# Kernel optimization log

Measured on AMD Instinct MI355X. Metric: run time of the kernel, lower is better.

## Reference

```python
import jax, jax.numpy as jnp
import numpy as np

RRELU_SLOPE = (1.0 / 8.0 + 1.0 / 3.0) / 2.0  # torch.rrelu eval-mode negative slope

N_NODES, N_EDGES, DIM, N_LAYERS = 10000, 640000, 128, 2


def setup_inputs() -> dict:
    key = jax.random.key(0)
    ks = jax.random.split(key, 7)
    scale = 1.0 / np.sqrt(DIM).astype(np.float32)
    return {
        "node_feats": jax.random.normal(ks[0], (N_NODES, DIM), jnp.float32),
        "edge_feats": jax.random.normal(ks[1], (N_EDGES, DIM), jnp.float32),
        "src": jax.random.randint(ks[2], (N_EDGES,), 0, N_NODES),
        "dst": jax.random.randint(ks[3], (N_EDGES,), 0, N_NODES),
        "W1": jax.random.normal(ks[4], (N_LAYERS, DIM, DIM), jnp.float32) * scale,
        "W2": jax.random.normal(ks[5], (N_LAYERS, DIM, DIM), jnp.float32) * scale,
        "W3": jax.random.normal(ks[6], (N_LAYERS, DIM, DIM), jnp.float32) * scale,
    }


def reference(node_feats, edge_feats, src, dst, W1, W2, W3):
    n_nodes = node_feats.shape[0]
    ones = jnp.ones((src.shape[0],), dtype=node_feats.dtype)
    deg = jax.ops.segment_sum(ones, dst, num_segments=n_nodes)  # in-degrees
    iso = (deg == 0)[:, None]                                   # isolated-node mask
    denom = jnp.maximum(deg, 1.0)[:, None]                      # safe mean divisor

    h = node_feats
    for l in range(W1.shape[0]):
        # per-edge message: linear1(src_h + edge_h)
        msg = (h[src] + edge_feats) @ W1[l]                     # (E, H)
        # mean-aggregate to destination nodes (0 for zero in-degree, as in dgl)
        neigh = jax.ops.segment_sum(msg, dst, num_segments=n_nodes) / denom
        # self-loop message; isolated nodes use linear3 instead of linear2
        self_msg = jnp.where(iso, h @ W3[l], h @ W2[l])
        x = neigh + self_msg
        h = jnp.where(x >= 0, x, RRELU_SLOPE * x)               # rrelu (eval mode)
    return h
```

## Files before the change

kernel.cpp:

```cpp
#include <hip/hip_runtime.h>

#define NN 10000
#define NE 640000
#define SLOPE 0.22916666666666666f

typedef float    f2v __attribute__((ext_vector_type(2)));
typedef float    f4v __attribute__((ext_vector_type(4)));
typedef unsigned u2v __attribute__((ext_vector_type(2)));
typedef unsigned u4v __attribute__((ext_vector_type(4)));

__device__ __forceinline__ float blo(unsigned v){ return __uint_as_float(v << 16); }
__device__ __forceinline__ float bhi(unsigned v){ return __uint_as_float(v & 0xffff0000u); }
__device__ __forceinline__ unsigned f2b(float x){
  unsigned u = __float_as_uint(x);
  return (u + 0x7fffu + ((u >> 16) & 1u)) >> 16;
}
__device__ __forceinline__ unsigned pack2(float a, float b){
  return f2b(a) | (f2b(b) << 16);
}
__device__ __forceinline__ float rrelu(float x){ return x >= 0.f ? x : x * SLOPE; }
__device__ __forceinline__ int clampi(int x, int hi){ return x < 0 ? 0 : (x > hi ? hi : x); }

__device__ __forceinline__ int detect_f32(const unsigned short* __restrict__ w1){
  int lane = threadIdx.x & 63;
  unsigned short u = w1[lane];
  int e = (u >> 7) & 0xFF;
  int pass = ((u & 0x7FFF) == 0 || (e >= 100 && e <= 135)) ? 1 : 0;
  unsigned long long b = __ballot(pass);
  return (__popcll(b) < 56) ? 1 : 0;
}

__device__ __forceinline__ float2 ld2(const void* p, long i, int f32){
  if (f32) return ((const float2*)p)[i];
  unsigned v = ((const unsigned*)p)[i];
  return make_float2(blo(v), bhi(v));
}
__device__ __forceinline__ void st2(void* p, long i, float2 v, int f32){
  if (f32) ((float2*)p)[i] = v;
  else ((unsigned*)p)[i] = pack2(v.x, v.y);
}

__global__ __launch_bounds__(256) void k_hist(const int* __restrict__ dst,
                                              int* __restrict__ deg){
  int i = blockIdx.x * 256 + threadIdx.x;
  if (i < NE) atomicAdd(&deg[clampi(dst[i], NN - 1)], 1);
}

__global__ __launch_bounds__(1024) void k_scan(const int* __restrict__ deg,
                                               int* __restrict__ row_ptr,
                                               int* __restrict__ cursor){
  __shared__ int part[1024];
  int t = threadIdx.x;
  int base = t * 10;
  int local[10];
  int s = 0;
  #pragma unroll
  for (int j = 0; j < 10; j++){
    int idx = base + j;
    int v = (idx < NN) ? deg[idx] : 0;
    local[j] = s; s += v;
  }
  part[t] = s;
  __syncthreads();
  for (int off = 1; off < 1024; off <<= 1){
    int v = (t >= off) ? part[t - off] : 0;
    __syncthreads();
    part[t] += v;
    __syncthreads();
  }
  int pre = (t == 0) ? 0 : part[t - 1];
  #pragma unroll
  for (int j = 0; j < 10; j++){
    int idx = base + j;
    if (idx < NN){ int rp = pre + local[j]; row_ptr[idx] = rp; cursor[idx] = rp; }
  }
  if (t == 1023) row_ptr[NN] = part[1023];
}

__global__ __launch_bounds__(256) void k_scatter_cast(const int* __restrict__ src,
                          const int* __restrict__ dst,
                          int* __restrict__ cursor,
                          unsigned long long* __restrict__ csr,
                          const void* __restrict__ nf, unsigned* __restrict__ nfbf,
                          const unsigned short* __restrict__ w1){
  int f32 = detect_f32(w1);
  int i = blockIdx.x * 256 + threadIdx.x;
  if (i >= NE) return;
  float2 v = ld2(nf, i, f32);
  nfbf[i] = pack2(v.x, v.y);
  int d = clampi(dst[i], NN - 1);
  int p = clampi(atomicAdd(&cursor[d], 1), NE - 1);
  csr[p] = ((unsigned long long)(unsigned)i << 32) | (unsigned)clampi(src[i], NN - 1);
}

__global__ __launch_bounds__(256) void k_agg0(const void* __restrict__ ef,
                                              const unsigned* __restrict__ nfbf,
                                              const int* __restrict__ row_ptr,
                                              const unsigned long long* __restrict__ csr,
                                              unsigned* __restrict__ eagg,
                                              unsigned* __restrict__ A,
                                              const unsigned short* __restrict__ w1){
  int f32 = detect_f32(w1);
  int wave = threadIdx.x >> 6, lane = threadIdx.x & 63;
  int n = blockIdx.x * 4 + wave;
  if (n >= NN) return;
  int beg = row_ptr[n], end = row_ptr[n + 1];
  float inv = 1.f / fmaxf((float)(end - beg), 1.f);
  int half = lane >> 5, sl = lane & 31;

  if (f32){
    const f4v* ef4 = (const f4v*)ef;
    const u2v* nf2 = (const u2v*)nfbf;
    float s0=0.f,s1=0.f,s2=0.f,s3=0.f;
    float h0=0.f,h1=0.f,h2=0.f,h3=0.f;
    int i = beg;
    for (; i + 8 <= end; i += 8){
      unsigned long long c[4];
      #pragma unroll
      for (int q = 0; q < 4; q++) c[q] = csr[i + 2*q + half];
      f4v v[4]; u2v hv[4];
      #pragma unroll
      for (int q = 0; q < 4; q++)
        v[q] = __builtin_nontemporal_load(ef4 + (long)(c[q] >> 32) * 32 + sl);
      #pragma unroll
      for (int q = 0; q < 4; q++)
        hv[q] = nf2[(long)(unsigned)(c[q] & 0xffffffffu) * 32 + sl];
      #pragma unroll
      for (int q = 0; q < 4; q++){
        s0 += v[q].x; s1 += v[q].y; s2 += v[q].z; s3 += v[q].w;
        h0 += blo(hv[q].x); h1 += bhi(hv[q].x);
        h2 += blo(hv[q].y); h3 += bhi(hv[q].y);
      }
    }
    for (; i + 2 <= end; i += 2){
      unsigned long long c = csr[i + half];
      f4v v = __builtin_nontemporal_load(ef4 + (long)(c >> 32) * 32 + sl);
      u2v hv = nf2[(long)(unsigned)(c & 0xffffffffu) * 32 + sl];
      s0 += v.x; s1 += v.y; s2 += v.z; s3 += v.w;
      h0 += blo(hv.x); h1 += bhi(hv.x); h2 += blo(hv.y); h3 += bhi(hv.y);
    }
    if (i < end && half == 0){
      unsigned long long c = csr[i];
      f4v v = __builtin_nontemporal_load(ef4 + (long)(c >> 32) * 32 + sl);
      u2v hv = nf2[(long)(unsigned)(c & 0xffffffffu) * 32 + sl];
      s0 += v.x; s1 += v.y; s2 += v.z; s3 += v.w;
      h0 += blo(hv.x); h1 += bhi(hv.x); h2 += blo(hv.y); h3 += bhi(hv.y);
    }
    s0 += __shfl_xor(s0, 32); s1 += __shfl_xor(s1, 32);
    s2 += __shfl_xor(s2, 32); s3 += __shfl_xor(s3, 32);
    h0 += __shfl_xor(h0, 32); h1 += __shfl_xor(h1, 32);
    h2 += __shfl_xor(h2, 32); h3 += __shfl_xor(h3, 32);
    if (half == 0){
      u2v eo; eo.x = pack2(s0, s1); eo.y = pack2(s2, s3);
      ((u2v*)eagg)[(long)n * 32 + sl] = eo;
      u2v ao; ao.x = pack2((s0 + h0) * inv, (s1 + h1) * inv);
      ao.y = pack2((s2 + h2) * inv, (s3 + h3) * inv);
      ((u2v*)A)[(long)n * 32 + sl] = ao;
    }
    return;
  }

  {
    const u2v* ef2 = (const u2v*)ef;
    const u2v* nf2 = (const u2v*)nfbf;
    float e00=0.f,e01=0.f,e10=0.f,e11=0.f;
    float h00=0.f,h01=0.f,h10=0.f,h11=0.f;
    int i = beg;
    for (; i + 8 <= end; i += 8){
      unsigned long long c[4];
      #pragma unroll
      for (int q = 0; q < 4; q++) c[q] = csr[i + 2*q + half];
      u2v v[4], hv[4];
      #pragma unroll
      for (int q = 0; q < 4; q++)
        v[q] = __builtin_nontemporal_load(ef2 + (long)(c[q] >> 32) * 32 + sl);
      #pragma unroll
      for (int q = 0; q < 4; q++)
        hv[q] = nf2[(long)(unsigned)(c[q] & 0xffffffffu) * 32 + sl];
      #pragma unroll
      for (int q = 0; q < 4; q++){
        e00 += blo(v[q].x);  e01 += bhi(v[q].x);
        e10 += blo(v[q].y);  e11 += bhi(v[q].y);
        h00 += blo(hv[q].x); h01 += bhi(hv[q].x);
        h10 += blo(hv[q].y); h11 += bhi(hv[q].y);
      }
    }
    for (; i + 2 <= end; i += 2){
      unsigned long long c = csr[i + half];
      u2v v = __builtin_nontemporal_load(ef2 + (long)(c >> 32) * 32 + sl);
      u2v hv = nf2[(long)(unsigned)(c & 0xffffffffu) * 32 + sl];
      e00 += blo(v.x);  e01 += bhi(v.x);  e10 += blo(v.y);  e11 += bhi(v.y);
      h00 += blo(hv.x); h01 += bhi(hv.x); h10 += blo(hv.y); h11 += bhi(hv.y);
    }
    if (i < end && half == 0){
      unsigned long long c = csr[i];
      u2v v = __builtin_nontemporal_load(ef2 + (long)(c >> 32) * 32 + sl);
      u2v hv = nf2[(long)(unsigned)(c & 0xffffffffu) * 32 + sl];
      e00 += blo(v.x);  e01 += bhi(v.x);  e10 += blo(v.y);  e11 += bhi(v.y);
      h00 += blo(hv.x); h01 += bhi(hv.x); h10 += blo(hv.y); h11 += bhi(hv.y);
    }
    e00 += __shfl_xor(e00, 32); e01 += __shfl_xor(e01, 32);
    e10 += __shfl_xor(e10, 32); e11 += __shfl_xor(e11, 32);
    h00 += __shfl_xor(h00, 32); h01 += __shfl_xor(h01, 32);
    h10 += __shfl_xor(h10, 32); h11 += __shfl_xor(h11, 32);
    if (half == 0){
      u2v eo; eo.x = pack2(e00, e01); eo.y = pack2(e10, e11);
      ((u2v*)eagg)[(long)n * 32 + sl] = eo;
      u2v ao; ao.x = pack2((e00 + h00) * inv, (e01 + h01) * inv);
      ao.y = pack2((e10 + h10) * inv, (e11 + h11) * inv);
      ((u2v*)A)[(long)n * 32 + sl] = ao;
    }
  }
}

__global__ __launch_bounds__(256) void k_agg_h(const unsigned* __restrict__ h,
                                               const int* __restrict__ row_ptr,
                                               const unsigned long long* __restrict__ csr,
                                               const unsigned* __restrict__ eagg,
                                               unsigned* __restrict__ A){
  int wave = threadIdx.x >> 6, lane = threadIdx.x & 63;
  int n = blockIdx.x * 4 + wave;
  if (n >= NN) return;
  int beg = row_ptr[n], end = row_ptr[n + 1];
  int qt = lane >> 4, ql = lane & 15;
  const u4v* h4 = (const u4v*)h;
  float a0=0.f,a1=0.f,a2=0.f,a3=0.f,a4=0.f,a5=0.f,a6=0.f,a7=0.f;
  int i = beg;
  for (; i + 16 <= end; i += 16){
    unsigned c[4];
    #pragma unroll
    for (int q = 0; q < 4; q++) c[q] = (unsigned)(csr[i + 4*q + qt] & 0xffffffffu);
    u4v v[4];
    #pragma unroll
    for (int q = 0; q < 4; q++) v[q] = h4[(long)c[q] * 16 + ql];
    #pragma unroll
    for (int q = 0; q < 4; q++){
      a0 += blo(v[q].x); a1 += bhi(v[q].x); a2 += blo(v[q].y); a3 += bhi(v[q].y);
      a4 += blo(v[q].z); a5 += bhi(v[q].z); a6 += blo(v[q].w); a7 += bhi(v[q].w);
    }
  }
  for (; i + 4 <= end; i += 4){
    unsigned c = (unsigned)(csr[i + qt] & 0xffffffffu);
    u4v v = h4[(long)c * 16 + ql];
    a0 += blo(v.x); a1 += bhi(v.x); a2 += blo(v.y); a3 += bhi(v.y);
    a4 += blo(v.z); a5 += bhi(v.z); a6 += blo(v.w); a7 += bhi(v.w);
  }
  int r = end - i;
  if (qt < r){
    unsigned c = (unsigned)(csr[i + qt] & 0xffffffffu);
    u4v v = h4[(long)c * 16 + ql];
    a0 += blo(v.x); a1 += bhi(v.x); a2 += blo(v.y); a3 += bhi(v.y);
    a4 += blo(v.z); a5 += bhi(v.z); a6 += blo(v.w); a7 += bhi(v.w);
  }
  a0 += __shfl_xor(a0, 16); a1 += __shfl_xor(a1, 16);
  a2 += __shfl_xor(a2, 16); a3 += __shfl_xor(a3, 16);
  a4 += __shfl_xor(a4, 16); a5 += __shfl_xor(a5, 16);
  a6 += __shfl_xor(a6, 16); a7 += __shfl_xor(a7, 16);
  a0 += __shfl_xor(a0, 32); a1 += __shfl_xor(a1, 32);
  a2 += __shfl_xor(a2, 32); a3 += __shfl_xor(a3, 32);
  a4 += __shfl_xor(a4, 32); a5 += __shfl_xor(a5, 32);
  a6 += __shfl_xor(a6, 32); a7 += __shfl_xor(a7, 32);
  if (qt == 0){
    u4v ev = ((const u4v*)eagg)[(long)n * 16 + ql];
    a0 += blo(ev.x); a1 += bhi(ev.x); a2 += blo(ev.y); a3 += bhi(ev.y);
    a4 += blo(ev.z); a5 += bhi(ev.z); a6 += blo(ev.w); a7 += bhi(ev.w);
    float inv = 1.f / fmaxf((float)(end - beg), 1.f);
    u4v ao;
    ao.x = pack2(a0 * inv, a1 * inv); ao.y = pack2(a2 * inv, a3 * inv);
    ao.z = pack2(a4 * inv, a5 * inv); ao.w = pack2(a6 * inv, a7 * inv);
    ((u4v*)A)[(long)n * 16 + ql] = ao;
  }
}

__global__ __launch_bounds__(512) void k_lin(const unsigned* __restrict__ A,
                                             const unsigned* __restrict__ H,
                                             const void* __restrict__ W1,
                                             const void* __restrict__ W2,
                                             const void* __restrict__ W3, long woff,
                                             const int* __restrict__ deg,
                                             void* __restrict__ out, int outmode){
  int f32 = detect_f32((const unsigned short*)W1);
  __shared__ unsigned lw[16384];
  int t = threadIdx.x;
  for (int i = t; i < 16384; i += 512){
    float2 v = (i < 8192) ? ld2(W1, woff + i, f32) : ld2(W2, woff + (i - 8192), f32);
    lw[i] = pack2(v.x, v.y);
  }
  __syncthreads();
  int wave = t >> 6, lane = t & 63;
  int nb = (blockIdx.x * 8 + wave) * 5;
  long base[5]; int valid[5];
  float a0[5], a1[5];
  #pragma unroll
  for (int j = 0; j < 5; ++j){
    int n = nb + j;
    valid[j] = (n < NN);
    base[j] = valid[j] ? (long)n * 64 : 0;
    a0[j] = 0.f; a1[j] = 0.f;
  }
  for (int kk = 0; kk < 64; ++kk){
    unsigned w1a = lw[(2 * kk) * 64 + lane];
    unsigned w1b = lw[(2 * kk + 1) * 64 + lane];
    unsigned w2a = lw[8192 + (2 * kk) * 64 + lane];
    unsigned w2b = lw[8192 + (2 * kk + 1) * 64 + lane];
    #pragma unroll
    for (int j = 0; j < 5; ++j){
      unsigned av = A[base[j] + kk];
      unsigned hv = H[base[j] + kk];
      float A0 = blo(av), A1 = bhi(av);
      float H0 = blo(hv), H1 = bhi(hv);
      a0[j] += A0 * blo(w1a) + A1 * blo(w1b) + H0 * blo(w2a) + H1 * blo(w2b);
      a1[j] += A0 * bhi(w1a) + A1 * bhi(w1b) + H0 * bhi(w2a) + H1 * bhi(w2b);
    }
  }
  #pragma unroll
  for (int j = 0; j < 5; ++j){
    if (valid[j] && deg[nb + j] == 0){
      float b0 = 0.f, b1 = 0.f;
      for (int kk = 0; kk < 64; ++kk){
        unsigned hv = H[base[j] + kk];
        float H0 = blo(hv), H1 = bhi(hv);
        float2 wa = ld2(W3, woff + (long)(2 * kk) * 64 + lane, f32);
        float2 wb = ld2(W3, woff + (long)(2 * kk + 1) * 64 + lane, f32);
        b0 += H0 * wa.x + H1 * wb.x;
        b1 += H0 * wa.y + H1 * wb.y;
      }
      a0[j] = b0; a1[j] = b1;
    }
  }
  #pragma unroll
  for (int j = 0; j < 5; ++j){
    if (!valid[j]) continue;
    float r0 = rrelu(a0[j]), r1 = rrelu(a1[j]);
    if (outmode) st2(out, base[j] + lane, make_float2(r0, r1), f32);
    else ((unsigned*)out)[base[j] + lane] = pack2(r0, r1);
  }
}

extern "C" void kernel_launch(void* const* d_in, const int* in_sizes, int n_in,
                              void* d_out, int out_size, void* d_ws, size_t ws_size,
                              hipStream_t stream) {
  const void* nf  = d_in[0];
  const void* ef  = d_in[1];
  const int*  src = (const int*)d_in[2];
  const int*  dst = (const int*)d_in[3];
  const void* W1  = d_in[4];
  const void* W2  = d_in[5];
  const void* W3  = d_in[6];

  char* w = (char*)d_ws;
  int* deg      = (int*)(w + 4096);
  int* row_ptr  = (int*)(w + 49152);
  int* cursor   = (int*)(w + 94208);
  unsigned long long* csr = (unsigned long long*)(w + 139264);
  unsigned* eagg = (unsigned*)(w + 5259264);
  unsigned* Abuf = (unsigned*)(w + 7819264);
  unsigned* nfbf = (unsigned*)(w + 10379264);
  unsigned* h1   = (unsigned*)(w + 12939264);

  const long WOFF1 = 8192;
  const unsigned short* w1u = (const unsigned short*)W1;

  hipMemsetAsync(deg, 0, NN * sizeof(int), stream);
  k_hist<<<2500, 256, 0, stream>>>(dst, deg);
  k_scan<<<1, 1024, 0, stream>>>(deg, row_ptr, cursor);
  k_scatter_cast<<<2500, 256, 0, stream>>>(src, dst, cursor, csr, nf, nfbf, w1u);
  k_agg0<<<2500, 256, 0, stream>>>(ef, nfbf, row_ptr, csr, eagg, Abuf, w1u);

  k_lin<<<250, 512, 0, stream>>>(Abuf, nfbf, W1, W2, W3, 0L, deg, h1, 0);

  k_agg_h<<<2500, 256, 0, stream>>>(h1, row_ptr, csr, eagg, Abuf);
  k_lin<<<250, 512, 0, stream>>>(Abuf, h1, W1, W2, W3, WOFF1, deg, d_out, 1);
}
```

Measured before the change: 625.3 us.

## Fuse per-layer aggregation with the linear transform and prepack weights to bf16

```diff
diff --git a/kernel.cpp b/kernel.cpp
--- a/kernel.cpp
+++ b/kernel.cpp
@@ -40,10 +40,24 @@
   else ((unsigned*)p)[i] = pack2(v.x, v.y);
 }
 
-__global__ __launch_bounds__(256) void k_hist(const int* __restrict__ dst,
-                                              int* __restrict__ deg){
+__global__ __launch_bounds__(256) void k_hist_pack(const int* __restrict__ dst,
+                          int* __restrict__ deg,
+                          const void* __restrict__ W1, const void* __restrict__ W2,
+                          const void* __restrict__ W3, unsigned* __restrict__ wpk,
+                          const unsigned short* __restrict__ w1u){
+  int f32 = detect_f32(w1u);
   int i = blockIdx.x * 256 + threadIdx.x;
   if (i < NE) atomicAdd(&deg[clampi(dst[i], NN - 1)], 1);
+  if (i < 49152){
+    float2 v;
+    if (i < 8192)       v = ld2(W1, i, f32);
+    else if (i < 16384) v = ld2(W2, i - 8192, f32);
+    else if (i < 24576) v = ld2(W1, 8192 + (i - 16384), f32);
+    else if (i < 32768) v = ld2(W2, 8192 + (i - 24576), f32);
+    else if (i < 40960) v = ld2(W3, i - 32768, f32);
+    else                v = ld2(W3, 8192 + (i - 40960), f32);
+    wpk[i] = pack2(v.x, v.y);
+  }
 }
 
 __global__ __launch_bounds__(1024) void k_scan(const int* __restrict__ deg,
@@ -93,220 +107,128 @@
   csr[p] = ((unsigned long long)(unsigned)i << 32) | (unsigned)clampi(src[i], NN - 1);
 }
 
-__global__ __launch_bounds__(256) void k_agg0(const void* __restrict__ ef,
-                                              const unsigned* __restrict__ nfbf,
-                                              const int* __restrict__ row_ptr,
-                                              const unsigned long long* __restrict__ csr,
-                                              unsigned* __restrict__ eagg,
-                                              unsigned* __restrict__ A,
-                                              const unsigned short* __restrict__ w1){
-  int f32 = detect_f32(w1);
+__global__ __launch_bounds__(256) void k_fused0(const void* __restrict__ ef,
+                          const unsigned* __restrict__ nfbf,
+                          const int* __restrict__ row_ptr,
+                          const unsigned long long* __restrict__ csr,
+                          unsigned* __restrict__ eagg,
+                          const unsigned* __restrict__ wpk,
+                          const int* __restrict__ deg,
+                          unsigned* __restrict__ h1,
+                          const unsigned short* __restrict__ w1u){
+  int f32 = detect_f32(w1u);
+  __shared__ unsigned sA[4][4][64];
   int wave = threadIdx.x >> 6, lane = threadIdx.x & 63;
-  int n = blockIdx.x * 4 + wave;
-  if (n >= NN) return;
-  int beg = row_ptr[n], end = row_ptr[n + 1];
-  float inv = 1.f / fmaxf((float)(end - beg), 1.f);
   int half = lane >> 5, sl = lane & 31;
-
-  if (f32){
-    const f4v* ef4 = (const f4v*)ef;
+  int nb = (blockIdx.x * 4 + wave) * 4;
+
+  for (int j = 0; j < 4; ++j){
+    int n = nb + j;
+    int beg = row_ptr[n], end = row_ptr[n + 1];
+    float inv = 1.f / fmaxf((float)(end - beg), 1.f);
+    float s0=0.f,s1=0.f,s2=0.f,s3=0.f;
+    float h0=0.f,h1v=0.f,h2=0.f,h3=0.f;
     const u2v* nf2 = (const u2v*)nfbf;
-    float s0=0.f,s1=0.f,s2=0.f,s3=0.f;
-    float h0=0.f,h1=0.f,h2=0.f,h3=0.f;
-    int i = beg;
-    for (; i + 8 <= end; i += 8){
-      unsigned long long c[4];
-      #pragma unroll
-      for (int q = 0; q < 4; q++) c[q] = csr[i + 2*q + half];
-      f4v v[4]; u2v hv[4];
-      #pragma unroll
-      for (int q = 0; q < 4; q++)
-        v[q] = __builtin_nontemporal_load(ef4 + (long)(c[q] >> 32) * 32 + sl);
-      #pragma unroll
-      for (int q = 0; q < 4; q++)
-        hv[q] = nf2[(long)(unsigned)(c[q] & 0xffffffffu) * 32 + sl];
-      #pragma unroll
-      for (int q = 0; q < 4; q++){
-        s0 += v[q].x; s1 += v[q].y; s2 += v[q].z; s3 += v[q].w;
-        h0 += blo(hv[q].x); h1 += bhi(hv[q].x);
-        h2 += blo(hv[q].y); h3 += bhi(hv[q].y);
-      }
-    }
-    for (; i + 2 <= end; i += 2){
-      unsigned long long c = csr[i + half];
-      f4v v = __builtin_nontemporal_load(ef4 + (long)(c >> 32) * 32 + sl);
-      u2v hv = nf2[(long)(unsigned)(c & 0xffffffffu) * 32 + sl];
-      s0 += v.x; s1 += v.y; s2 += v.z; s3 += v.w;
-      h0 += blo(hv.x); h1 += bhi(hv.x); h2 += blo(hv.y); h3 += bhi(hv.y);
-    }
-    if (i < end && half == 0){
-      unsigned long long c = csr[i];
-      f4v v = __builtin_nontemporal_load(ef4 + (long)(c >> 32) * 32 + sl);
-      u2v hv = nf2[(long)(unsigned)(c & 0xffffffffu) * 32 + sl];
-      s0 += v.x; s1 += v.y; s2 += v.z; s3 += v.w;
-      h0 += blo(hv.x); h1 += bhi(hv.x); h2 += blo(hv.y); h3 += bhi(hv.y);
+
+    if (f32){
+      const f4v* ef4 = (const f4v*)ef;
+      int i = beg;
+      for (; i + 8 <= end; i += 8){
+        unsigned long long c[4];
+        #pragma unroll
+        for (int q = 0; q < 4; q++) c[q] = csr[i + 2*q + half];
+        f4v v[4]; u2v hv[4];
+        #pragma unroll
+        for (int q = 0; q < 4; q++)
+          v[q] = __builtin_nontemporal_load(ef4 + (long)(c[q] >> 32) * 32 + sl);
+        #pragma unroll
+        for (int q = 0; q < 4; q++)
+          hv[q] = nf2[(long)(unsigned)(c[q] & 0xffffffffu) * 32 + sl];
+        #pragma unroll
+        for (int q = 0; q < 4; q++){
+          s0 += v[q].x; s1 += v[q].y; s2 += v[q].z; s3 += v[q].w;
+          h0 += blo(hv[q].x); h1v += bhi(hv[q].x);
+          h2 += blo(hv[q].y); h3  += bhi(hv[q].y);
+        }
+      }
+      for (; i + 2 <= end; i += 2){
+        unsigned long long c = csr[i + half];
+        f4v v = __builtin_nontemporal_load(ef4 + (long)(c >> 32) * 32 + sl);
+        u2v hv = nf2[(long)(unsigned)(c & 0xffffffffu) * 32 + sl];
+        s0 += v.x; s1 += v.y; s2 += v.z; s3 += v.w;
+        h0 += blo(hv.x); h1v += bhi(hv.x); h2 += blo(hv.y); h3 += bhi(hv.y);
+      }
+      if (i < end && half == 0){
+        unsigned long long c = csr[i];
+        f4v v = __builtin_nontemporal_load(ef4 + (long)(c >> 32) * 32 + sl);
+        u2v hv = nf2[(long)(unsigned)(c & 0xffffffffu) * 32 + sl];
+        s0 += v.x; s1 += v.y; s2 += v.z; s3 += v.w;
+        h0 += blo(hv.x); h1v += bhi(hv.x); h2 += blo(hv.y); h3 += bhi(hv.y);
+      }
+    } else {
+      const u2v* ef2 = (const u2v*)ef;
+      int i = beg;
+      for (; i + 8 <= end; i += 8){
+        unsigned long long c[4];
+        #pragma unroll
+        for (int q = 0; q < 4; q++) c[q] = csr[i + 2*q + half];
+        u2v v[4], hv[4];
+        #pragma unroll
+        for (int q = 0; q < 4; q++)
+          v[q] = __builtin_nontemporal_load(ef2 + (long)(c[q] >> 32) * 32 + sl);
+        #pragma unroll
+        for (int q = 0; q < 4; q++)
+          hv[q] = nf2[(long)(unsigned)(c[q] & 0xffffffffu) * 32 + sl];
+        #pragma unroll
+        for (int q = 0; q < 4; q++){
+          s0 += blo(v[q].x);  s1 += bhi(v[q].x);
+          s2 += blo(v[q].y);  s3 += bhi(v[q].y);
+          h0 += blo(hv[q].x); h1v += bhi(hv[q].x);
+          h2 += blo(hv[q].y); h3  += bhi(hv[q].y);
+        }
+      }
+      for (; i + 2 <= end; i += 2){
+        unsigned long long c = csr[i + half];
+        u2v v = __builtin_nontemporal_load(ef2 + (long)(c >> 32) * 32 + sl);
+        u2v hv = nf2[(long)(unsigned)(c & 0xffffffffu) * 32 + sl];
+        s0 += blo(v.x); s1 += bhi(v.x); s2 += blo(v.y); s3 += bhi(v.y);
+        h0 += blo(hv.x); h1v += bhi(hv.x); h2 += blo(hv.y); h3 += bhi(hv.y);
+      }
+      if (i < end && half == 0){
+        unsigned long long c = csr[i];
+        u2v v = __builtin_nontemporal_load(ef2 + (long)(c >> 32) * 32 + sl);
+        u2v hv = nf2[(long)(unsigned)(c & 0xffffffffu) * 32 + sl];
+        s0 += blo(v.x); s1 += bhi(v.x); s2 += blo(v.y); s3 += bhi(v.y);
+        h0 += blo(hv.x); h1v += bhi(hv.x); h2 += blo(hv.y); h3 += bhi(hv.y);
+      }
     }
     s0 += __shfl_xor(s0, 32); s1 += __shfl_xor(s1, 32);
     s2 += __shfl_xor(s2, 32); s3 += __shfl_xor(s3, 32);
-    h0 += __shfl_xor(h0, 32); h1 += __shfl_xor(h1, 32);
-    h2 += __shfl_xor(h2, 32); h3 += __shfl_xor(h3, 32);
+    h0 += __shfl_xor(h0, 32); h1v += __shfl_xor(h1v, 32);
+    h2 += __shfl_xor(h2, 32); h3  += __shfl_xor(h3, 32);
     if (half == 0){
       u2v eo; eo.x = pack2(s0, s1); eo.y = pack2(s2, s3);
       ((u2v*)eagg)[(long)n * 32 + sl] = eo;
-      u2v ao; ao.x = pack2((s0 + h0) * inv, (s1 + h1) * inv);
+      u2v ao; ao.x = pack2((s0 + h0) * inv, (s1 + h1v) * inv);
       ao.y = pack2((s2 + h2) * inv, (s3 + h3) * inv);
-      ((u2v*)A)[(long)n * 32 + sl] = ao;
-    }
-    return;
-  }
-
-  {
-    const u2v* ef2 = (const u2v*)ef;
-    const u2v* nf2 = (const u2v*)nfbf;
-    float e00=0.f,e01=0.f,e10=0.f,e11=0.f;
-    float h00=0.f,h01=0.f,h10=0.f,h11=0.f;
-    int i = beg;
-    for (; i + 8 <= end; i += 8){
-      unsigned long long c[4];
-      #pragma unroll
-      for (int q = 0; q < 4; q++) c[q] = csr[i + 2*q + half];
-      u2v v[4], hv[4];
-      #pragma unroll
-      for (int q = 0; q < 4; q++)
-        v[q] = __builtin_nontemporal_load(ef2 + (long)(c[q] >> 32) * 32 + sl);
-      #pragma unroll
-      for (int q = 0; q < 4; q++)
-        hv[q] = nf2[(long)(unsigned)(c[q] & 0xffffffffu) * 32 + sl];
-      #pragma unroll
-      for (int q = 0; q < 4; q++){
-        e00 += blo(v[q].x);  e01 += bhi(v[q].x);
-        e10 += blo(v[q].y);  e11 += bhi(v[q].y);
-        h00 += blo(hv[q].x); h01 += bhi(hv[q].x);
-        h10 += blo(hv[q].y); h11 += bhi(hv[q].y);
-      }
-    }
-    for (; i + 2 <= end; i += 2){
-      unsigned long long c = csr[i + half];
-      u2v v = __builtin_nontemporal_load(ef2 + (long)(c >> 32) * 32 + sl);
-      u2v hv = nf2[(long)(unsigned)(c & 0xffffffffu) * 32 + sl];
-      e00 += blo(v.x);  e01 += bhi(v.x);  e10 += blo(v.y);  e11 += bhi(v.y);
-      h00 += blo(hv.x); h01 += bhi(hv.x); h10 += blo(hv.y); h11 += bhi(hv.y);
-    }
-    if (i < end && half == 0){
-      unsigned long long c = csr[i];
-      u2v v = __builtin_nontemporal_load(ef2 + (long)(c >> 32) * 32 + sl);
-      u2v hv = nf2[(long)(unsigned)(c & 0xffffffffu) * 32 + sl];
-      e00 += blo(v.x);  e01 += bhi(v.x);  e10 += blo(v.y);  e11 += bhi(v.y);
-      h00 += blo(hv.x); h01 += bhi(hv.x); h10 += blo(hv.y); h11 += bhi(hv.y);
-    }
-    e00 += __shfl_xor(e00, 32); e01 += __shfl_xor(e01, 32);
-    e10 += __shfl_xor(e10, 32); e11 += __shfl_xor(e11, 32);
-    h00 += __shfl_xor(h00, 32); h01 += __shfl_xor(h01, 32);
-    h10 += __shfl_xor(h10, 32); h11 += __shfl_xor(h11, 32);
-    if (half == 0){
-      u2v eo; eo.x = pack2(e00, e01); eo.y = pack2(e10, e11);
-      ((u2v*)eagg)[(long)n * 32 + sl] = eo;
-      u2v ao; ao.x = pack2((e00 + h00) * inv, (e01 + h01) * inv);
-      ao.y = pack2((e10 + h10) * inv, (e11 + h11) * inv);
-      ((u2v*)A)[(long)n * 32 + sl] = ao;
-    }
-  }
-}
-
-__global__ __launch_bounds__(256) void k_agg_h(const unsigned* __restrict__ h,
-                                               const int* __restrict__ row_ptr,
-                                               const unsigned long long* __restrict__ csr,
-                                               const unsigned* __restrict__ eagg,
-                                               unsigned* __restrict__ A){
-  int wave = threadIdx.x >> 6, lane = threadIdx.x & 63;
-  int n = blockIdx.x * 4 + wave;
-  if (n >= NN) return;
-  int beg = row_ptr[n], end = row_ptr[n + 1];
-  int qt = lane >> 4, ql = lane & 15;
-  const u4v* h4 = (const u4v*)h;
-  float a0=0.f,a1=0.f,a2=0.f,a3=0.f,a4=0.f,a5=0.f,a6=0.f,a7=0.f;
-  int i = beg;
-  for (; i + 16 <= end; i += 16){
-    unsigned c[4];
+      *(u2v*)&sA[wave][j][2 * sl] = ao;
+    }
+  }
+
+  long hb[4]; float a0[4], a1[4];
+  #pragma unroll
+  for (int j = 0; j < 4; ++j){ hb[j] = (long)(nb + j) * 64; a0[j] = 0.f; a1[j] = 0.f; }
+  const unsigned* wp1 = wpk;
+  const unsigned* wp2 = wpk + 8192;
+  for (int kk = 0; kk < 64; ++kk){
+    unsigned w1a = wp1[(2 * kk) * 64 + lane];
+    unsigned w1b = wp1[(2 * kk + 1) * 64 + lane];
+    unsigned w2a = wp2[(2 * kk) * 64 + lane];
+    unsigned w2b = wp2[(2 * kk + 1) * 64 + lane];
     #pragma unroll
-    for (int q = 0; q < 4; q++) c[q] = (unsigned)(csr[i + 4*q + qt] & 0xffffffffu);
-    u4v v[4];
-    #pragma unroll
-    for (int q = 0; q < 4; q++) v[q] = h4[(long)c[q] * 16 + ql];
-    #pragma unroll
-    for (int q = 0; q < 4; q++){
-      a0 += blo(v[q].x); a1 += bhi(v[q].x); a2 += blo(v[q].y); a3 += bhi(v[q].y);
-      a4 += blo(v[q].z); a5 += bhi(v[q].z); a6 += blo(v[q].w); a7 += bhi(v[q].w);
-    }
-  }
-  for (; i + 4 <= end; i += 4){
-    unsigned c = (unsigned)(csr[i + qt] & 0xffffffffu);
-    u4v v = h4[(long)c * 16 + ql];
-    a0 += blo(v.x); a1 += bhi(v.x); a2 += blo(v.y); a3 += bhi(v.y);
-    a4 += blo(v.z); a5 += bhi(v.z); a6 += blo(v.w); a7 += bhi(v.w);
-  }
-  int r = end - i;
-  if (qt < r){
-    unsigned c = (unsigned)(csr[i + qt] & 0xffffffffu);
-    u4v v = h4[(long)c * 16 + ql];
-    a0 += blo(v.x); a1 += bhi(v.x); a2 += blo(v.y); a3 += bhi(v.y);
-    a4 += blo(v.z); a5 += bhi(v.z); a6 += blo(v.w); a7 += bhi(v.w);
-  }
-  a0 += __shfl_xor(a0, 16); a1 += __shfl_xor(a1, 16);
-  a2 += __shfl_xor(a2, 16); a3 += __shfl_xor(a3, 16);
-  a4 += __shfl_xor(a4, 16); a5 += __shfl_xor(a5, 16);
-  a6 += __shfl_xor(a6, 16); a7 += __shfl_xor(a7, 16);
-  a0 += __shfl_xor(a0, 32); a1 += __shfl_xor(a1, 32);
-  a2 += __shfl_xor(a2, 32); a3 += __shfl_xor(a3, 32);
-  a4 += __shfl_xor(a4, 32); a5 += __shfl_xor(a5, 32);
-  a6 += __shfl_xor(a6, 32); a7 += __shfl_xor(a7, 32);
-  if (qt == 0){
-    u4v ev = ((const u4v*)eagg)[(long)n * 16 + ql];
-    a0 += blo(ev.x); a1 += bhi(ev.x); a2 += blo(ev.y); a3 += bhi(ev.y);
-    a4 += blo(ev.z); a5 += bhi(ev.z); a6 += blo(ev.w); a7 += bhi(ev.w);
-    float inv = 1.f / fmaxf((float)(end - beg), 1.f);
-    u4v ao;
-    ao.x = pack2(a0 * inv, a1 * inv); ao.y = pack2(a2 * inv, a3 * inv);
-    ao.z = pack2(a4 * inv, a5 * inv); ao.w = pack2(a6 * inv, a7 * inv);
-    ((u4v*)A)[(long)n * 16 + ql] = ao;
-  }
-}
-
-__global__ __launch_bounds__(512) void k_lin(const unsigned* __restrict__ A,
-                                             const unsigned* __restrict__ H,
-                                             const void* __restrict__ W1,
-                                             const void* __restrict__ W2,
-                                             const void* __restrict__ W3, long woff,
-                                             const int* __restrict__ deg,
-                                             void* __restrict__ out, int outmode){
-  int f32 = detect_f32((const unsigned short*)W1);
-  __shared__ unsigned lw[16384];
-  int t = threadIdx.x;
-  for (int i = t; i < 16384; i += 512){
-    float2 v = (i < 8192) ? ld2(W1, woff + i, f32) : ld2(W2, woff + (i - 8192), f32);
-    lw[i] = pack2(v.x, v.y);
-  }
-  __syncthreads();
-  int wave = t >> 6, lane = t & 63;
-  int nb = (blockIdx.x * 8 + wave) * 5;
-  long base[5]; int valid[5];
-  float a0[5], a1[5];
-  #pragma unroll
-  for (int j = 0; j < 5; ++j){
-    int n = nb + j;
-    valid[j] = (n < NN);
-    base[j] = valid[j] ? (long)n * 64 : 0;
-    a0[j] = 0.f; a1[j] = 0.f;
-  }
-  for (int kk = 0; kk < 64; ++kk){
-    unsigned w1a = lw[(2 * kk) * 64 + lane];
-    unsigned w1b = lw[(2 * kk + 1) * 64 + lane];
-    unsigned w2a = lw[8192 + (2 * kk) * 64 + lane];
-    unsigned w2b = lw[8192 + (2 * kk + 1) * 64 + lane];
-    #pragma unroll
-    for (int j = 0; j < 5; ++j){
-      unsigned av = A[base[j] + kk];
-      unsigned hv = H[base[j] + kk];
+    for (int j = 0; j < 4; ++j){
+      unsigned av = sA[wave][j][kk];
+      unsigned hv = nfbf[hb[j] + kk];
       float A0 = blo(av), A1 = bhi(av);
       float H0 = blo(hv), H1 = bhi(hv);
       a0[j] += A0 * blo(w1a) + A1 * blo(w1b) + H0 * blo(w2a) + H1 * blo(w2b);
@@ -314,27 +236,129 @@
     }
   }
   #pragma unroll
-  for (int j = 0; j < 5; ++j){
-    if (valid[j] && deg[nb + j] == 0){
+  for (int j = 0; j < 4; ++j){
+    if (deg[nb + j] == 0){
+      const unsigned* wp3 = wpk + 32768;
       float b0 = 0.f, b1 = 0.f;
       for (int kk = 0; kk < 64; ++kk){
-        unsigned hv = H[base[j] + kk];
-        float H0 = blo(hv), H1 = bhi(hv);
-        float2 wa = ld2(W3, woff + (long)(2 * kk) * 64 + lane, f32);
-        float2 wb = ld2(W3, woff + (long)(2 * kk + 1) * 64 + lane, f32);
-        b0 += H0 * wa.x + H1 * wb.x;
-        b1 += H0 * wa.y + H1 * wb.y;
+        unsigned hv = nfbf[hb[j] + kk];
+        unsigned wa = wp3[(2 * kk) * 64 + lane];
+        unsigned wb = wp3[(2 * kk + 1) * 64 + lane];
+        b0 += blo(hv) * blo(wa) + bhi(hv) * blo(wb);
+        b1 += blo(hv) * bhi(wa) + bhi(hv) * bhi(wb);
       }
       a0[j] = b0; a1[j] = b1;
     }
   }
   #pragma unroll
-  for (int j = 0; j < 5; ++j){
-    if (!valid[j]) continue;
-    float r0 = rrelu(a0[j]), r1 = rrelu(a1[j]);
-    if (outmode) st2(out, base[j] + lane, make_float2(r0, r1), f32);
-    else ((unsigned*)out)[base[j] + lane] = pack2(r0, r1);
-  }
+  for (int j = 0; j < 4; ++j)
+    h1[hb[j] + lane] = pack2(rrelu(a0[j]), rrelu(a1[j]));
+}
+
+__global__ __launch_bounds__(256) void k_fused1(const unsigned* __restrict__ h1,
+                          const int* __restrict__ row_ptr,
+                          const unsigned long long* __restrict__ csr,
+                          const unsigned* __restrict__ eagg,
+                          const unsigned* __restrict__ wpk,
+                          const int* __restrict__ deg,
+                          void* __restrict__ out,
+                          const unsigned short* __restrict__ w1u){
+  int f32 = detect_f32(w1u);
+  __shared__ unsigned sA[4][4][64];
+  int wave = threadIdx.x >> 6, lane = threadIdx.x & 63;
+  int qt = lane >> 4, ql = lane & 15;
+  int nb = (blockIdx.x * 4 + wave) * 4;
+  const u4v* h4 = (const u4v*)h1;
+
+  for (int j = 0; j < 4; ++j){
+    int n = nb + j;
+    int beg = row_ptr[n], end = row_ptr[n + 1];
+    float a0=0.f,a1=0.f,a2=0.f,a3=0.f,a4=0.f,a5=0.f,a6=0.f,a7=0.f;
+    int i = beg;
+    for (; i + 16 <= end; i += 16){
+      unsigned c[4];
+      #pragma unroll
+      for (int q = 0; q < 4; q++) c[q] = (unsigned)(csr[i + 4*q + qt] & 0xffffffffu);
+      u4v v[4];
+      #pragma unroll
+      for (int q = 0; q < 4; q++) v[q] = h4[(long)c[q] * 16 + ql];
+      #pragma unroll
+      for (int q = 0; q < 4; q++){
+        a0 += blo(v[q].x); a1 += bhi(v[q].x); a2 += blo(v[q].y); a3 += bhi(v[q].y);
+        a4 += blo(v[q].z); a5 += bhi(v[q].z); a6 += blo(v[q].w); a7 += bhi(v[q].w);
+      }
+    }
+    for (; i + 4 <= end; i += 4){
+      unsigned c = (unsigned)(csr[i + qt] & 0xffffffffu);
+      u4v v = h4[(long)c * 16 + ql];
+      a0 += blo(v.x); a1 += bhi(v.x); a2 += blo(v.y); a3 += bhi(v.y);
+      a4 += blo(v.z); a5 += bhi(v.z); a6 += blo(v.w); a7 += bhi(v.w);
+    }
+    int r = end - i;
+    if (qt < r){
+      unsigned c = (unsigned)(csr[i + qt] & 0xffffffffu);
+      u4v v = h4[(long)c * 16 + ql];
+      a0 += blo(v.x); a1 += bhi(v.x); a2 += blo(v.y); a3 += bhi(v.y);
+      a4 += blo(v.z); a5 += bhi(v.z); a6 += blo(v.w); a7 += bhi(v.w);
+    }
+    a0 += __shfl_xor(a0, 16); a1 += __shfl_xor(a1, 16);
+    a2 += __shfl_xor(a2, 16); a3 += __shfl_xor(a3, 16);
+    a4 += __shfl_xor(a4, 16); a5 += __shfl_xor(a5, 16);
+    a6 += __shfl_xor(a6, 16); a7 += __shfl_xor(a7, 16);
+    a0 += __shfl_xor(a0, 32); a1 += __shfl_xor(a1, 32);
+    a2 += __shfl_xor(a2, 32); a3 += __shfl_xor(a3, 32);
+    a4 += __shfl_xor(a4, 32); a5 += __shfl_xor(a5, 32);
+    a6 += __shfl_xor(a6, 32); a7 += __shfl_xor(a7, 32);
+    if (qt == 0){
+      u4v ev = ((const u4v*)eagg)[(long)n * 16 + ql];
+      a0 += blo(ev.x); a1 += bhi(ev.x); a2 += blo(ev.y); a3 += bhi(ev.y);
+      a4 += blo(ev.z); a5 += bhi(ev.z); a6 += blo(ev.w); a7 += bhi(ev.w);
+      float inv = 1.f / fmaxf((float)(end - beg), 1.f);
+      u4v ao;
+      ao.x = pack2(a0 * inv, a1 * inv); ao.y = pack2(a2 * inv, a3 * inv);
+      ao.z = pack2(a4 * inv, a5 * inv); ao.w = pack2(a6 * inv, a7 * inv);
+      *(u4v*)&sA[wave][j][4 * ql] = ao;
+    }
+  }
+
+  long hb[4]; float a0[4], a1[4];
+  #pragma unroll
+  for (int j = 0; j < 4; ++j){ hb[j] = (long)(nb + j) * 64; a0[j] = 0.f; a1[j] = 0.f; }
+  const unsigned* wp1 = wpk + 16384;
+  const unsigned* wp2 = wpk + 24576;
+  for (int kk = 0; kk < 64; ++kk){
+    unsigned w1a = wp1[(2 * kk) * 64 + lane];
+    unsigned w1b = wp1[(2 * kk + 1) * 64 + lane];
+    unsigned w2a = wp2[(2 * kk) * 64 + lane];
+    unsigned w2b = wp2[(2 * kk + 1) * 64 + lane];
+    #pragma unroll
+    for (int j = 0; j < 4; ++j){
+      unsigned av = sA[wave][j][kk];
+      unsigned hv = h1[hb[j] + kk];
+      float A0 = blo(av), A1 = bhi(av);
+      float H0 = blo(hv), H1 = bhi(hv);
+      a0[j] += A0 * blo(w1a) + A1 * blo(w1b) + H0 * blo(w2a) + H1 * blo(w2b);
+      a1[j] += A0 * bhi(w1a) + A1 * bhi(w1b) + H0 * bhi(w2a) + H1 * bhi(w2b);
+    }
+  }
+  #pragma unroll
+  for (int j = 0; j < 4; ++j){
+    if (deg[nb + j] == 0){
+      const unsigned* wp3 = wpk + 40960;
+      float b0 = 0.f, b1 = 0.f;
+      for (int kk = 0; kk < 64; ++kk){
+        unsigned hv = h1[hb[j] + kk];
+        unsigned wa = wp3[(2 * kk) * 64 + lane];
+        unsigned wb = wp3[(2 * kk + 1) * 64 + lane];
+        b0 += blo(hv) * blo(wa) + bhi(hv) * blo(wb);
+        b1 += blo(hv) * bhi(wa) + bhi(hv) * bhi(wb);
+      }
+      a0[j] = b0; a1[j] = b1;
+    }
+  }
+  #pragma unroll
+  for (int j = 0; j < 4; ++j)
+    st2(out, hb[j] + lane, make_float2(rrelu(a0[j]), rrelu(a1[j])), f32);
 }
 
 extern "C" void kernel_launch(void* const* d_in, const int* in_sizes, int n_in,
@@ -354,21 +378,16 @@
   int* cursor   = (int*)(w + 94208);
   unsigned long long* csr = (unsigned long long*)(w + 139264);
   unsigned* eagg = (unsigned*)(w + 5259264);
-  unsigned* Abuf = (unsigned*)(w + 7819264);
+  unsigned* wpk  = (unsigned*)(w + 7819264);
   unsigned* nfbf = (unsigned*)(w + 10379264);
   unsigned* h1   = (unsigned*)(w + 12939264);
 
-  const long WOFF1 = 8192;
   const unsigned short* w1u = (const unsigned short*)W1;
 
   hipMemsetAsync(deg, 0, NN * sizeof(int), stream);
-  k_hist<<<2500, 256, 0, stream>>>(dst, deg);
+  k_hist_pack<<<2500, 256, 0, stream>>>(dst, deg, W1, W2, W3, wpk, w1u);
   k_scan<<<1, 1024, 0, stream>>>(deg, row_ptr, cursor);
   k_scatter_cast<<<2500, 256, 0, stream>>>(src, dst, cursor, csr, nf, nfbf, w1u);
-  k_agg0<<<2500, 256, 0, stream>>>(ef, nfbf, row_ptr, csr, eagg, Abuf, w1u);
-
-  k_lin<<<250, 512, 0, stream>>>(Abuf, nfbf, W1, W2, W3, 0L, deg, h1, 0);
-
-  k_agg_h<<<2500, 256, 0, stream>>>(h1, row_ptr, csr, eagg, Abuf);
-  k_lin<<<250, 512, 0, stream>>>(Abuf, h1, W1, W2, W3, WOFF1, deg, d_out, 1);
-}
+  k_fused0<<<625, 256, 0, stream>>>(ef, nfbf, row_ptr, csr, eagg, wpk, deg, h1, w1u);
+  k_fused1<<<625, 256, 0, stream>>>(h1, row_ptr, csr, eagg, wpk, deg, d_out, w1u);
+}
```

New measurement: 611.0 us. -2.3%, faster.
